# Optimization experiments

Hardware: AMD Instinct MI355X
Metric: run time of the kernel (lower is better)

Reference implementation:

```python
import math
import jax, jax.numpy as jnp
from jax import lax
import numpy as np

PATCHES = [(8, 8), (4, 4), (2, 2), (1, 1)]  # (width, height) per scale
BN_EPS = 1e-5


def setup_inputs() -> dict:
    key = jax.random.key(0)
    ks = jax.random.split(key, 9)
    b, d, h, w = 4, 256, 64, 64
    s = 1.0 / math.sqrt(d)
    return {
        "x": jax.random.normal(ks[0], (b, d, h, w), jnp.float32),
        "wq": jax.random.normal(ks[1], (d, d), jnp.float32) * s,
        "bq": jax.random.normal(ks[2], (d,), jnp.float32) * 0.02,
        "wk": jax.random.normal(ks[3], (d, d), jnp.float32) * s,
        "bk": jax.random.normal(ks[4], (d,), jnp.float32) * 0.02,
        "wv": jax.random.normal(ks[5], (d, d), jnp.float32) * s,
        "bv": jax.random.normal(ks[6], (d,), jnp.float32) * 0.02,
        "w_out": jax.random.normal(ks[7], (d, d, 3, 3), jnp.float32) * (s / 3.0),
        "b_out": jax.random.normal(ks[8], (d,), jnp.float32) * 0.02,
        "gamma": jnp.ones((d,), jnp.float32),
        "beta": jnp.zeros((d,), jnp.float32),
    }


def _to_tokens(t, b, dk, out_h, ph, out_w, pw):
    # [b, dk, h, w] -> [b, out_h*out_w, dk*ph*pw]
    t = t.reshape(b, dk, out_h, ph, out_w, pw)
    t = t.transpose(0, 2, 4, 1, 3, 5)
    return t.reshape(b, out_h * out_w, dk * ph * pw)


def reference(x, wq, bq, wk, bk, wv, bv, w_out, b_out, gamma, beta):
    b, c, h, w = x.shape
    # 1x1 conv projections == channel matmuls
    q = jnp.einsum('bchw,oc->bohw', x, wq) + bq[None, :, None, None]
    k = jnp.einsum('bchw,oc->bohw', x, wk) + bk[None, :, None, None]
    v = jnp.einsum('bchw,oc->bohw', x, wv) + bv[None, :, None, None]

    dk = c // len(PATCHES)
    outs = []
    for i, (pw, ph) in enumerate(PATCHES):
        sl = slice(i * dk, (i + 1) * dk)
        out_h, out_w = h // ph, w // pw
        Q = _to_tokens(q[:, sl], b, dk, out_h, ph, out_w, pw)
        K = _to_tokens(k[:, sl], b, dk, out_h, ph, out_w, pw)
        V = _to_tokens(v[:, sl], b, dk, out_h, ph, out_w, pw)
        scores = jnp.einsum('bnd,bmd->bnm', Q, K) / math.sqrt(Q.shape[-1])
        p = jax.nn.softmax(scores, axis=-1)
        y = jnp.einsum('bnm,bmd->bnd', p, V)
        # tokens -> [b, dk, h, w]
        y = y.reshape(b, out_h, out_w, dk, ph, pw)
        y = y.transpose(0, 3, 1, 4, 2, 5).reshape(b, dk, h, w)
        outs.append(y)
    out = jnp.concatenate(outs, axis=1)

    # 3x3 conv, padding=1
    z = lax.conv_general_dilated(out, w_out, (1, 1), 'SAME',
                                 dimension_numbers=('NCHW', 'OIHW', 'NCHW'))
    z = z + b_out[None, :, None, None]
    # BatchNorm2d (training-mode batch stats)
    mean = jnp.mean(z, axis=(0, 2, 3), keepdims=True)
    var = jnp.var(z, axis=(0, 2, 3), keepdims=True)
    zn = (z - mean) * lax.rsqrt(var + BN_EPS)
    zn = zn * gamma[None, :, None, None] + beta[None, :, None, None]
    # LeakyReLU(0.2)
    return jnp.where(zn > 0, zn, 0.2 * zn)
```

## Files before the change

kernel.cpp:

```cpp
#include <hip/hip_runtime.h>
#include <cmath>


#define OFF_XB  0LL
#define OFF_QB  2097152LL
#define OFF_SS  8388608LL
#define OFF_PP  12582912LL
#define OFF_YT  14680064LL
#define OFF_WQK 18874368LL
#define OFF_BIA 18972672LL
#define OFF_WCV 18973440LL
#define OFF_STT 19268352LL
#define OFF_SP0 19268864LL
#define OFF_S1  19399936LL
#define OFF_P0  19662080LL
#define OFF_P1  19670272LL

#define FC 0.18033688f
#define CSHIFT 6.0f

typedef __attribute__((ext_vector_type(8))) short short8;
typedef __attribute__((ext_vector_type(4))) float f32x4;

__device__ inline unsigned short f2bf(float f) {
  unsigned u = __float_as_uint(f);
  u += 0x7fff + ((u >> 16) & 1);
  return (unsigned short)(u >> 16);
}

__device__ inline unsigned cvt_pk_bf16(float a, float b) {
  unsigned r;
  asm("v_cvt_pk_bf16_f32 %0, %1, %2" : "=v"(r) : "v"(a), "v"(b));
  return r;
}

__global__ __launch_bounds__(256) void prep_k(
    const float* __restrict__ x, unsigned short* __restrict__ xb,
    const float* __restrict__ wq, const float* __restrict__ wk,
    const float* __restrict__ wv, const float* __restrict__ bq,
    const float* __restrict__ bk, const float* __restrict__ bv,
    unsigned short* __restrict__ Wqkv, float* __restrict__ biasQKV,
    const float* __restrict__ wcv, unsigned short* __restrict__ Wcb)
{
  const int bid = blockIdx.x, t = threadIdx.x;
  if (bid < 256) {
    __shared__ unsigned short rowb[256][66];
    const int b = bid >> 6, y = bid & 63;
    for (int i = t; i < 16384; i += 256) {
      int c = i >> 6, xx = i & 63;
      rowb[c][xx] = f2bf(x[((long long)(b*256 + c) << 12) + (y << 6) + xx]);
    }
    __syncthreads();
    unsigned int* outw = (unsigned int*)(xb + ((long long)bid << 14));
    for (int i = t; i < 8192; i += 256) {
      int xx = i >> 7, c2 = (i & 127) * 2;
      outw[xx*128 + (c2 >> 1)] = (unsigned)rowb[c2][xx]
                               | ((unsigned)rowb[c2+1][xx] << 16);
    }
  } else if (bid < 1024) {
    const int row = bid - 256;
    const int which = row >> 8, oc = row & 255;
    const float* src = which == 0 ? wq : which == 1 ? wk : wv;
    Wqkv[row*256 + t] = f2bf(src[oc*256 + t]);
    if (row < 3) {
      const float* bs = row == 0 ? bq : row == 1 ? bk : bv;
      biasQKV[row*256 + t] = bs[t];
    }
  } else {
    int i = (bid - 1024)*256 + t;
    int tap = i >> 16, oc = (i >> 8) & 255, ic = i & 255;
    Wcb[i] = f2bf(wcv[((long long)(oc*256 + ic))*9 + tap]);
  }
}

template<int EPI, int SH = 0>
__device__ void gemm_nt_body(
    const unsigned short* __restrict__ A, const unsigned short* __restrict__ B,
    void* __restrict__ Cv, const float* __restrict__ bias,
    int M, int N, int K, int lda, int ldb, int ldc,
    long long sA, long long sB, long long sC, float alpha,
    int bx, int by, int bz)
{
  const int t = threadIdx.x, l = t & 63;
  const int lr = l & 15, lg = l >> 4;
  const int w = t >> 6, wm = w >> 1, wn = w & 1;
  const int m0 = by*128 + wm*64, n0 = bx*128 + wn*64;
  if (m0 >= M || n0 >= N) return;
  const unsigned short* Ab = A + (long long)bz*sA + (long long)(m0 + lr)*lda + lg*8;
  const unsigned short* Bb = B + (long long)bz*sB + (long long)(n0 + lr)*ldb + lg*8;

  f32x4 acc[4][4] = {};
#pragma unroll 2
  for (int kk = 0; kk < K; kk += 32) {
    short8 af[4], bf[4];
#pragma unroll
    for (int i = 0; i < 4; i++)
      af[i] = *(const short8*)(Ab + (long long)i*16*lda + kk);
#pragma unroll
    for (int i = 0; i < 4; i++)
      bf[i] = *(const short8*)(Bb + (long long)i*16*ldb + kk);
#pragma unroll
    for (int mf = 0; mf < 4; mf++)
#pragma unroll
      for (int nf = 0; nf < 4; nf++)
        acc[mf][nf] = __builtin_amdgcn_mfma_f32_16x16x32_bf16(
            af[mf], bf[nf], acc[mf][nf], 0, 0, 0);
  }

  if (EPI == 0) {
    float* C = (float*)Cv + (long long)bz*sC;
#pragma unroll
    for (int mf = 0; mf < 4; mf++)
#pragma unroll
      for (int r = 0; r < 4; r++) {
        const int row = m0 + mf*16 + lg*4 + r;
#pragma unroll
        for (int nf = 0; nf < 4; nf++)
          C[(long long)row*ldc + n0 + nf*16 + lr] = acc[mf][nf][r] * alpha;
      }
  } else if (EPI == 1) {
    unsigned short* Qbase = (unsigned short*)Cv;
#pragma unroll
    for (int mf = 0; mf < 4; mf++)
#pragma unroll
      for (int r = 0; r < 4; r++) {
        const int gi = m0 + mf*16 + lg*4 + r;
        const int which = gi >> 8, ch = gi & 255;
        const int scale = ch >> 6, c = ch & 63;
        const int sh = 3 - scale, msk = (1 << sh) - 1;
        const bool tr = (which == 2);
        const float bb = bias[gi];
        unsigned short* dst = Qbase + (long long)which*4194304
                            + (long long)scale*1048576 + (long long)bz*262144;
#pragma unroll
        for (int nf = 0; nf < 4; nf++) {
          const int gj = n0 + nf*16 + lr;
          const int y = gj >> 6, xx = gj & 63;
          const int n = (y >> sh)*(64 >> sh) + (xx >> sh);
          const int d = (c << (2*sh)) + ((y & msk) << sh) + (xx & msk);
          const long long idx = tr
              ? (long long)d*(4096 >> (2*sh)) + n
              : (long long)n*(64 << (2*sh)) + d;
          dst[idx] = f2bf(acc[mf][nf][r] + bb);
        }
      }
  } else {
    unsigned short* inb = (unsigned short*)Cv;
    constexpr int msk = (1 << SH) - 1;
    constexpr int scale = 3 - SH;
#pragma unroll
    for (int mf = 0; mf < 4; mf++)
#pragma unroll
      for (int r = 0; r < 4; r++) {
        const int gi = m0 + mf*16 + lg*4 + r;
        const int ty = gi >> (6 - SH), tx = gi & ((64 >> SH) - 1);
#pragma unroll
        for (int nf = 0; nf < 4; nf++) {
          const int gj = n0 + nf*16 + lr;
          const int c = gj >> (2*SH);
          const int y = (ty << SH) | ((gj >> SH) & msk);
          const int x = (tx << SH) | (gj & msk);
          inb[((((long long)bz << 12) + (y << 6) + x) << 8) + scale*64 + c]
              = f2bf(acc[mf][nf][r]);
        }
      }
  }
}

__global__ __launch_bounds__(256) void qkv_k(
    const unsigned short* __restrict__ Wqkv, const unsigned short* __restrict__ xb,
    unsigned short* __restrict__ Qu, const float* __restrict__ biasQKV)
{
  gemm_nt_body<1>(Wqkv, xb, (void*)Qu, biasQKV, 768, 4096, 256, 256, 256, 0,
                  0, 1048576, 0, 1.0f, blockIdx.x, blockIdx.y, blockIdx.z);
}

__device__ void s0_scores_wave(
    const unsigned short* __restrict__ Q, const unsigned short* __restrict__ K,
    float* __restrict__ Sp, int bid)
{
  const int t = threadIdx.x, l = t & 63, w = t >> 6;
  const int lr = l & 15, lg = l >> 4;
  const int task = bid*4 + w;
  const int b = task >> 3, ks = task & 7;
  const unsigned short* Qb = Q + (long long)b*262144;
  const unsigned short* Kb = K + (long long)b*262144;
  f32x4 acc[4][4] = {};
  const int k0 = ks*512;
#pragma unroll 2
  for (int kk = k0; kk < k0 + 512; kk += 32) {
    short8 af[4], bf[4];
#pragma unroll
    for (int i = 0; i < 4; i++)
      af[i] = *(const short8*)(Qb + (long long)(i*16 + lr)*4096 + kk + lg*8);
#pragma unroll
    for (int i = 0; i < 4; i++)
      bf[i] = *(const short8*)(Kb + (long long)(i*16 + lr)*4096 + kk + lg*8);
#pragma unroll
    for (int mf = 0; mf < 4; mf++)
#pragma unroll
      for (int nf = 0; nf < 4; nf++)
        acc[mf][nf] = __builtin_amdgcn_mfma_f32_16x16x32_bf16(
            af[mf], bf[nf], acc[mf][nf], 0, 0, 0);
  }
#pragma unroll
  for (int mf = 0; mf < 4; mf++)
#pragma unroll
    for (int r = 0; r < 4; r++) {
      const int row = mf*16 + lg*4 + r;
#pragma unroll
      for (int nf = 0; nf < 4; nf++)
        Sp[(((long long)(ks*4 + b)*64 + row) << 6) + nf*16 + lr]
            = acc[mf][nf][r];
    }
}

__device__ void flash3_body(
    const unsigned short* __restrict__ Q3, const unsigned short* __restrict__ K3,
    const unsigned short* __restrict__ Vt3, unsigned short* __restrict__ inb,
    int bx, int b)
{
  constexpr int LD = 72;
  __shared__ unsigned short KVs[2][2][64*LD];
  __shared__ unsigned short Ps[64*LD];
  const int t = threadIdx.x, l = t & 63, w = t >> 6;
  const int lr = l & 15, lg = l >> 4;
  const int q0 = bx * 64;
  const long long base = (long long)b * 262144;
  const unsigned short* Qg = Q3 + base;
  const unsigned short* Kg = K3 + base;
  const unsigned short* Vg = Vt3 + base;

  short8 bq[2];
  bq[0] = *(const short8*)(Qg + (long long)(q0 + w*16 + lr)*64 + lg*8);
  bq[1] = *(const short8*)(Qg + (long long)(q0 + w*16 + lr)*64 + 32 + lg*8);

  f32x4 acc[4] = {};
  float li = 0.f;

  const int r_ = t >> 3, c8_ = (t & 7) * 8;
  uint4 kreg[2], vreg[2];

#define LOADKV(KT) do { \
    const int k0_ = (KT) * 64; \
    _Pragma("unroll") \
    for (int it = 0; it < 2; it++) { \
      const int rr = r_ + it*32; \
      kreg[it] = *(const uint4*)(Kg + (long long)(k0_ + rr)*64 + c8_); \
      vreg[it] = *(const uint4*)(Vg + (long long)rr*4096 + k0_ + c8_); \
    } } while (0)
#define STOREKV(BUF) do { \
    _Pragma("unroll") \
    for (int it = 0; it < 2; it++) { \
      const int rr = r_ + it*32; \
      *(uint4*)(KVs[BUF][0] + rr*LD + c8_) = kreg[it]; \
      *(uint4*)(KVs[BUF][1] + rr*LD + c8_) = vreg[it]; \
    } } while (0)

  LOADKV(0);
  STOREKV(0);
  __syncthreads();

  for (int kt = 0; kt < 64; ++kt) {
    if (kt < 63) LOADKV(kt + 1);
    const unsigned short* Ksb = KVs[kt & 1][0];
    const unsigned short* Vsb = KVs[kt & 1][1];
    f32x4 s[4];
#pragma unroll
    for (int cf = 0; cf < 4; cf++) {
      short8 ak0 = *(const short8*)(Ksb + (cf*16 + lr)*LD + lg*8);
      short8 ak1 = *(const short8*)(Ksb + (cf*16 + lr)*LD + 32 + lg*8);
      f32x4 zz = {};
      zz = __builtin_amdgcn_mfma_f32_16x16x32_bf16(ak0, bq[0], zz, 0,0,0);
      s[cf] = __builtin_amdgcn_mfma_f32_16x16x32_bf16(ak1, bq[1], zz, 0,0,0);
    }
    float p[16], psum = 0.f;
#pragma unroll
    for (int cf = 0; cf < 4; cf++)
#pragma unroll
      for (int r = 0; r < 4; r++) {
        float e = exp2f(fmaf(s[cf][r], FC, -CSHIFT));
        p[cf*4 + r] = e; psum += e;
      }
    li += psum;
    {
      unsigned short* pr = Ps + (w*16 + lr)*LD;
#pragma unroll
      for (int cf = 0; cf < 4; cf++) {
        *(unsigned*)(pr + cf*16 + lg*4)     = cvt_pk_bf16(p[cf*4+0], p[cf*4+1]);
        *(unsigned*)(pr + cf*16 + lg*4 + 2) = cvt_pk_bf16(p[cf*4+2], p[cf*4+3]);
      }
    }
    short8 bp0 = *(const short8*)(Ps + (w*16 + lr)*LD + lg*8);
    short8 bp1 = *(const short8*)(Ps + (w*16 + lr)*LD + 32 + lg*8);
#pragma unroll
    for (int df = 0; df < 4; df++) {
      short8 av0 = *(const short8*)(Vsb + (df*16 + lr)*LD + lg*8);
      short8 av1 = *(const short8*)(Vsb + (df*16 + lr)*LD + 32 + lg*8);
      acc[df] = __builtin_amdgcn_mfma_f32_16x16x32_bf16(av0, bp0, acc[df], 0,0,0);
      acc[df] = __builtin_amdgcn_mfma_f32_16x16x32_bf16(av1, bp1, acc[df], 0,0,0);
    }
    if (kt < 63) {
      STOREKV((kt + 1) & 1);
      __syncthreads();
    }
  }
#undef LOADKV
#undef STOREKV
  li += __shfl_xor(li, 16);
  li += __shfl_xor(li, 32);
  const float inv = 1.f / li;
  const long long row = (long long)b*4096 + q0 + w*16 + lr;
  unsigned short* ob = inb + row*256 + 192 + lg*4;
#pragma unroll
  for (int df = 0; df < 4; df++) {
    *(unsigned*)(ob + df*16)     = cvt_pk_bf16(acc[df][0]*inv, acc[df][1]*inv);
    *(unsigned*)(ob + df*16 + 2) = cvt_pk_bf16(acc[df][2]*inv, acc[df][3]*inv);
  }
}

__global__ __launch_bounds__(256) void stageA_k(
    const unsigned short* __restrict__ Qu, const unsigned short* __restrict__ Ku,
    const unsigned short* __restrict__ Vu,
    float* __restrict__ Sp0, float* __restrict__ S1, float* __restrict__ S2,
    unsigned short* __restrict__ inb)
{
  const int bid = blockIdx.x;
  if (bid < 256) {
    flash3_body(Qu+3145728, Ku+3145728, Vu+3145728, inb, bid & 63, bid >> 6);
  } else if (bid < 264) {
    s0_scores_wave(Qu, Ku, Sp0, bid - 256);
  } else if (bid < 280) {
    int q = bid - 264;
    gemm_nt_body<0>(Qu+1048576, Ku+1048576, (void*)S1, nullptr,
        256, 256, 1024, 1024, 1024, 256, 262144, 262144, 65536, 0.03125f,
        q & 1, (q >> 1) & 1, q >> 2);
  } else {
    int q = bid - 280;
    gemm_nt_body<0>(Qu+2097152, Ku+2097152, (void*)S2, nullptr,
        1024, 1024, 256, 256, 256, 1024, 262144, 262144, 1048576, 0.0625f,
        q & 7, (q >> 3) & 7, q >> 6);
  }
}

template<int CNT>
__device__ void softmax_row(const float* __restrict__ S,
                            unsigned short* __restrict__ P, long long row)
{
  const int l = threadIdx.x & 63;
  const float* p = S + row*(CNT*64);
  unsigned short* o = P + row*(CNT*64);
  float v[CNT];
  float mx = -1e30f;
#pragma unroll
  for (int i = 0; i < CNT; i++) { v[i] = p[i*64 + l]; mx = fmaxf(mx, v[i]); }
#pragma unroll
  for (int off = 1; off < 64; off <<= 1) mx = fmaxf(mx, __shfl_xor(mx, off, 64));
  float sum = 0.f;
#pragma unroll
  for (int i = 0; i < CNT; i++) { v[i] = __expf(v[i] - mx); sum += v[i]; }
#pragma unroll
  for (int off = 1; off < 64; off <<= 1) sum += __shfl_xor(sum, off, 64);
  const float inv = 1.f / sum;
#pragma unroll
  for (int i = 0; i < CNT; i++) o[i*64 + l] = f2bf(v[i] * inv);
}

__global__ __launch_bounds__(256) void stageB_k(
    const float* __restrict__ Sp0, unsigned short* __restrict__ P0,
    const float* __restrict__ S1, unsigned short* __restrict__ P1,
    const float* __restrict__ S2, unsigned short* __restrict__ P2)
{
  const int bid = blockIdx.x, t = threadIdx.x, l = t & 63, w = t >> 6;
  if (bid < 1024) {
    softmax_row<16>(S2, P2, (long long)bid*4 + w);
  } else if (bid < 1280) {
    softmax_row<4>(S1, P1, (long long)(bid - 1024)*4 + w);
  } else {
    const int row = (bid - 1280)*4 + w;
    const int b = row >> 6, r = row & 63;
    float v = 0.f;
#pragma unroll
    for (int ks = 0; ks < 8; ks++)
      v += Sp0[(((long long)(ks*4 + b)*64 + r) << 6) + l];
    v *= 0.015625f;
    float mx = v;
#pragma unroll
    for (int off = 1; off < 64; off <<= 1) mx = fmaxf(mx, __shfl_xor(mx, off, 64));
    float e = __expf(v - mx), sum = e;
#pragma unroll
    for (int off = 1; off < 64; off <<= 1) sum += __shfl_xor(sum, off, 64);
    P0[(row << 6) + l] = f2bf(e / sum);
  }
}

__global__ __launch_bounds__(256) void stageC_k(
    const unsigned short* __restrict__ P0, const unsigned short* __restrict__ P1,
    const unsigned short* __restrict__ P2, const unsigned short* __restrict__ Vu,
    unsigned short* __restrict__ inb)
{
  const int bid = blockIdx.x;
  if (bid < 128) {
    int q = bid;
    gemm_nt_body<2,3>(P0, Vu, (void*)inb, nullptr,
        64, 4096, 64, 64, 64, 0, 4096, 262144, 0, 1.0f,
        q & 31, 0, q >> 5);
  } else if (bid < 192) {
    int q = bid - 128;
    gemm_nt_body<2,2>(P1, Vu+1048576, (void*)inb, nullptr,
        256, 1024, 256, 256, 256, 0, 65536, 262144, 0, 1.0f,
        q & 7, (q >> 3) & 1, q >> 4);
  } else {
    int q = bid - 192;
    gemm_nt_body<2,1>(P2, Vu+2097152, (void*)inb, nullptr,
        1024, 256, 1024, 1024, 1024, 0, 1048576, 262144, 0, 1.0f,
        q & 1, (q >> 1) & 7, q >> 4);
  }
}

__global__ __launch_bounds__(512) void conv_mfma_k(
    const unsigned short* __restrict__ inb, const unsigned short* __restrict__ Wb,
    const float* __restrict__ bias, float* __restrict__ z)
{
  __shared__ unsigned short lds[2][6*66*32];
  const int t = threadIdx.x;
  const int l = t & 63, wid = t >> 6;
  const int lr = l & 15, lg = l >> 4;
  const int waveM = wid >> 2, waveN = wid & 3;
  const int b = blockIdx.x >> 4, y0 = (blockIdx.x & 15) * 4;
  const int oc0 = blockIdx.y * 64 + waveM * 32;
  const long long inbase = (long long)b * 1048576;
  const int kgrp = lg * 8;

  f32x4 acc[2][4] = {};
  uint4 sreg[4];

#define CLOAD(IC0) do { \
    _Pragma("unroll") \
    for (int i = 0; i < 4; i++) { \
      int q = t + i*512; \
      if (q < 1584) { \
        int ic8 = q & 3, cc = (q >> 2) % 66, rr = q / 264; \
        int gy = y0 - 1 + rr, gx = cc - 1; \
        uint4 v = make_uint4(0u,0u,0u,0u); \
        if ((unsigned)gy < 64u && (unsigned)gx < 64u) \
          v = *(const uint4*)(inb + inbase + ((long long)(gy*64+gx))*256 \
                              + (IC0) + ic8*8); \
        sreg[i] = v; \
      } \
    } } while (0)
#define CSTORE(BUF) do { \
    _Pragma("unroll") \
    for (int i = 0; i < 4; i++) { \
      int q = t + i*512; \
      if (q < 1584) *(uint4*)(&lds[BUF][q*8]) = sreg[i]; \
    } } while (0)

  CLOAD(0);
  CSTORE(0);
  __syncthreads();

  for (int c = 0; c < 8; ++c) {
    const int ic0 = c * 32;
    if (c < 7) CLOAD(ic0 + 32);
    const unsigned short* wbase = Wb + (long long)(oc0 + lr)*256 + ic0 + kgrp;
    short8 afr[9][2];
#pragma unroll
    for (int tap = 0; tap < 9; tap++) {
      afr[tap][0] = *(const short8*)(wbase + (long long)tap*65536);
      afr[tap][1] = *(const short8*)(wbase + (long long)tap*65536 + 16*256);
    }
    const unsigned short* L = lds[c & 1];
#pragma unroll
    for (int ky = 0; ky < 3; ky++) {
#pragma unroll
      for (int kx = 0; kx < 3; kx++) {
        const int tap = ky*3 + kx;
#pragma unroll
        for (int nf = 0; nf < 4; nf++) {
          int pix = waveN*64 + nf*16 + lr;
          int rp = pix >> 6, xx = pix & 63;
          short8 bf = *(const short8*)(L + ((rp + ky)*66 + xx + kx)*32 + kgrp);
          acc[0][nf] = __builtin_amdgcn_mfma_f32_16x16x32_bf16(
              afr[tap][0], bf, acc[0][nf], 0, 0, 0);
          acc[1][nf] = __builtin_amdgcn_mfma_f32_16x16x32_bf16(
              afr[tap][1], bf, acc[1][nf], 0, 0, 0);
        }
      }
    }
    if (c < 7) {
      CSTORE((c + 1) & 1);
      __syncthreads();
    }
  }
#undef CLOAD
#undef CSTORE

  const long long zb = ((long long)b * 256) << 12;
#pragma unroll
  for (int mf = 0; mf < 2; mf++) {
#pragma unroll
    for (int r = 0; r < 4; r++) {
      const int oc = oc0 + mf*16 + lg*4 + r;
      const float bb = bias[oc];
      const long long rowbase = zb + ((long long)oc << 12) + y0*64;
#pragma unroll
      for (int nf = 0; nf < 4; nf++) {
        int pix = waveN*64 + nf*16 + lr;
        z[rowbase + pix] = acc[mf][nf][r] + bb;
      }
    }
  }
}

__global__ __launch_bounds__(256) void bn_stats_k(
    const float* __restrict__ z, float* __restrict__ stats)
{
  const int ch = blockIdx.x, t = threadIdx.x;
  float s = 0.f, q = 0.f;
  for (int b = 0; b < 4; b++) {
    const float* p = z + ((long long)(b*256 + ch) << 12);
    for (int i = t; i < 4096; i += 256) { float v = p[i]; s += v; q += v*v; }
  }
  __shared__ float rs[256], rq[256];
  rs[t] = s; rq[t] = q; __syncthreads();
  for (int st = 128; st > 0; st >>= 1) {
    if (t < st) { rs[t] += rs[t+st]; rq[t] += rq[t+st]; }
    __syncthreads();
  }
  if (t == 0) {
    float mean = rs[0] * (1.f/16384.f);
    float var  = rq[0] * (1.f/16384.f) - mean*mean;
    stats[ch]       = mean;
    stats[256 + ch] = rsqrtf(var + 1e-5f);
  }
}

__global__ __launch_bounds__(256) void bn_apply_k(
    const float* __restrict__ z, const float* __restrict__ stats,
    const float* __restrict__ gamma, const float* __restrict__ beta,
    float* __restrict__ out)
{
  long long i4 = ((long long)blockIdx.x*256 + threadIdx.x) * 4;
  int ch = (int)((i4 >> 12) & 255);
  float mean = stats[ch], rsg = stats[256 + ch];
  float g = gamma[ch], bt = beta[ch];
  float4 v = *(const float4*)(z + i4);
  float r[4] = {v.x, v.y, v.z, v.w};
#pragma unroll
  for (int j = 0; j < 4; j++) {
    float u = (r[j] - mean) * rsg * g + bt;
    r[j] = u > 0.f ? u : 0.2f * u;
  }
  *(float4*)(out + i4) = make_float4(r[0], r[1], r[2], r[3]);
}

extern "C" void kernel_launch(void* const* d_in, const int* in_sizes, int n_in,
                              void* d_out, int out_size, void* d_ws, size_t ws_size,
                              hipStream_t stream)
{
  const float* x     = (const float*)d_in[0];
  const float* wq    = (const float*)d_in[1];
  const float* bq    = (const float*)d_in[2];
  const float* wk    = (const float*)d_in[3];
  const float* bk    = (const float*)d_in[4];
  const float* wv    = (const float*)d_in[5];
  const float* bv    = (const float*)d_in[6];
  const float* w_out = (const float*)d_in[7];
  const float* b_out = (const float*)d_in[8];
  const float* gamma = (const float*)d_in[9];
  const float* beta  = (const float*)d_in[10];
  float* out = (float*)d_out;

  float* ws = (float*)d_ws;
  unsigned short* xb  = (unsigned short*)(ws + OFF_XB);
  unsigned short* Qu  = (unsigned short*)(ws + OFF_QB);
  unsigned short* Ku  = Qu + 4194304;
  unsigned short* Vu  = Qu + 8388608;
  float* S2  = ws + OFF_SS;
  unsigned short* P2 = (unsigned short*)(ws + OFF_PP);
  unsigned short* Wqk = (unsigned short*)(ws + OFF_WQK);
  float* biasQ = ws + OFF_BIA;
  unsigned short* Wcv = (unsigned short*)(ws + OFF_WCV);
  float* St  = ws + OFF_STT;
  float* Sp0 = ws + OFF_SP0;
  float* S1  = ws + OFF_S1;
  unsigned short* P0 = (unsigned short*)(ws + OFF_P0);
  unsigned short* P1 = (unsigned short*)(ws + OFF_P1);
  unsigned short* inb = (unsigned short*)(ws + OFF_XB);
  float* z = ws + OFF_YT;

  dim3 blk(256);

  prep_k<<<dim3(3328), blk, 0, stream>>>(
      x, xb, wq, wk, wv, bq, bk, bv, Wqk, biasQ, w_out, Wcv);

  qkv_k<<<dim3(32,6,4), blk, 0, stream>>>(Wqk, xb, Qu, biasQ);

  stageA_k<<<dim3(536), blk, 0, stream>>>(Qu, Ku, Vu, Sp0, S1, S2, inb);

  stageB_k<<<dim3(1344), blk, 0, stream>>>(Sp0, P0, S1, P1, S2, P2);

  stageC_k<<<dim3(256), blk, 0, stream>>>(P0, P1, P2, Vu, inb);

  conv_mfma_k<<<dim3(64,4), dim3(512), 0, stream>>>(inb, Wcv, b_out, z);

  bn_stats_k<<<dim3(256), blk, 0, stream>>>(z, St);
  bn_apply_k<<<dim3(4096), blk, 0, stream>>>(z, St, gamma, beta, out);
}
```

Before: 234.3 us.

## Split flash attention keys across four wave groups per block with LDS reduction

The scale-3 flash attention blocks grow from 4 to 16 waves. Each group of 4 waves handles a quarter of the key range, so each wave runs 16 tile iterations instead of 64. Because the softmax uses a fixed exponent shift rather than a running max, partial accumulators and row sums can simply be added. Groups 1-3 write their partials to shared memory and group 0 adds them up and writes the output. This drops the register double-buffered K/V prefetch in favour of plain load-sync-compute steps, and uses much more LDS. Blocks of the other stage-A kinds now launch 1024 threads but exit the extra 768 immediately.

```diff
diff --git a/kernel.cpp b/kernel.cpp
--- a/kernel.cpp
+++ b/kernel.cpp
@@ -221,10 +221,12 @@
     int bx, int b)
 {
   constexpr int LD = 72;
-  __shared__ unsigned short KVs[2][2][64*LD];
-  __shared__ unsigned short Ps[64*LD];
+  __shared__ unsigned short KV4[4][2][64*LD];
+  __shared__ unsigned short Ps4[4][64*LD];
+  __shared__ float liC[192];
   const int t = threadIdx.x, l = t & 63, w = t >> 6;
   const int lr = l & 15, lg = l >> 4;
+  const int grp = w >> 2, sw = w & 3;
   const int q0 = bx * 64;
   const long long base = (long long)b * 262144;
   const unsigned short* Qg = Q3 + base;
@@ -232,44 +234,35 @@
   const unsigned short* Vg = Vt3 + base;
 
   short8 bq[2];
-  bq[0] = *(const short8*)(Qg + (long long)(q0 + w*16 + lr)*64 + lg*8);
-  bq[1] = *(const short8*)(Qg + (long long)(q0 + w*16 + lr)*64 + 32 + lg*8);
+  bq[0] = *(const short8*)(Qg + (long long)(q0 + sw*16 + lr)*64 + lg*8);
+  bq[1] = *(const short8*)(Qg + (long long)(q0 + sw*16 + lr)*64 + 32 + lg*8);
 
   f32x4 acc[4] = {};
   float li = 0.f;
 
-  const int r_ = t >> 3, c8_ = (t & 7) * 8;
-  uint4 kreg[2], vreg[2];
-
-#define LOADKV(KT) do { \
-    const int k0_ = (KT) * 64; \
-    _Pragma("unroll") \
-    for (int it = 0; it < 2; it++) { \
-      const int rr = r_ + it*32; \
-      kreg[it] = *(const uint4*)(Kg + (long long)(k0_ + rr)*64 + c8_); \
-      vreg[it] = *(const uint4*)(Vg + (long long)rr*4096 + k0_ + c8_); \
-    } } while (0)
-#define STOREKV(BUF) do { \
-    _Pragma("unroll") \
-    for (int it = 0; it < 2; it++) { \
-      const int rr = r_ + it*32; \
-      *(uint4*)(KVs[BUF][0] + rr*LD + c8_) = kreg[it]; \
-      *(uint4*)(KVs[BUF][1] + rr*LD + c8_) = vreg[it]; \
-    } } while (0)
-
-  LOADKV(0);
-  STOREKV(0);
-  __syncthreads();
-
-  for (int kt = 0; kt < 64; ++kt) {
-    if (kt < 63) LOADKV(kt + 1);
-    const unsigned short* Ksb = KVs[kt & 1][0];
-    const unsigned short* Vsb = KVs[kt & 1][1];
+  unsigned short* Ks = KV4[grp][0];
+  unsigned short* Vs = KV4[grp][1];
+  unsigned short* Ps = Ps4[grp];
+  const int tg = t & 255;
+  const int r_ = tg >> 3, c8_ = (tg & 7) * 8;
+
+  for (int i = 0; i < 16; i++) {
+    const int k0 = (grp*16 + i) * 64;
+    __syncthreads();
+#pragma unroll
+    for (int it = 0; it < 2; it++) {
+      const int rr = r_ + it*32;
+      *(uint4*)(Ks + rr*LD + c8_) =
+          *(const uint4*)(Kg + (long long)(k0 + rr)*64 + c8_);
+      *(uint4*)(Vs + rr*LD + c8_) =
+          *(const uint4*)(Vg + (long long)rr*4096 + k0 + c8_);
+    }
+    __syncthreads();
     f32x4 s[4];
 #pragma unroll
     for (int cf = 0; cf < 4; cf++) {
-      short8 ak0 = *(const short8*)(Ksb + (cf*16 + lr)*LD + lg*8);
-      short8 ak1 = *(const short8*)(Ksb + (cf*16 + lr)*LD + 32 + lg*8);
+      short8 ak0 = *(const short8*)(Ks + (cf*16 + lr)*LD + lg*8);
+      short8 ak1 = *(const short8*)(Ks + (cf*16 + lr)*LD + 32 + lg*8);
       f32x4 zz = {};
       zz = __builtin_amdgcn_mfma_f32_16x16x32_bf16(ak0, bq[0], zz, 0,0,0);
       s[cf] = __builtin_amdgcn_mfma_f32_16x16x32_bf16(ak1, bq[1], zz, 0,0,0);
@@ -284,42 +277,59 @@
       }
     li += psum;
     {
-      unsigned short* pr = Ps + (w*16 + lr)*LD;
+      unsigned short* pr = Ps + (sw*16 + lr)*LD;
 #pragma unroll
       for (int cf = 0; cf < 4; cf++) {
         *(unsigned*)(pr + cf*16 + lg*4)     = cvt_pk_bf16(p[cf*4+0], p[cf*4+1]);
         *(unsigned*)(pr + cf*16 + lg*4 + 2) = cvt_pk_bf16(p[cf*4+2], p[cf*4+3]);
       }
     }
-    short8 bp0 = *(const short8*)(Ps + (w*16 + lr)*LD + lg*8);
-    short8 bp1 = *(const short8*)(Ps + (w*16 + lr)*LD + 32 + lg*8);
+    short8 bp0 = *(const short8*)(Ps + (sw*16 + lr)*LD + lg*8);
+    short8 bp1 = *(const short8*)(Ps + (sw*16 + lr)*LD + 32 + lg*8);
 #pragma unroll
     for (int df = 0; df < 4; df++) {
-      short8 av0 = *(const short8*)(Vsb + (df*16 + lr)*LD + lg*8);
-      short8 av1 = *(const short8*)(Vsb + (df*16 + lr)*LD + 32 + lg*8);
+      short8 av0 = *(const short8*)(Vs + (df*16 + lr)*LD + lg*8);
+      short8 av1 = *(const short8*)(Vs + (df*16 + lr)*LD + 32 + lg*8);
       acc[df] = __builtin_amdgcn_mfma_f32_16x16x32_bf16(av0, bp0, acc[df], 0,0,0);
       acc[df] = __builtin_amdgcn_mfma_f32_16x16x32_bf16(av1, bp1, acc[df], 0,0,0);
     }
-    if (kt < 63) {
-      STOREKV((kt + 1) & 1);
-      __syncthreads();
-    }
-  }
-#undef LOADKV
-#undef STOREKV
+  }
   li += __shfl_xor(li, 16);
   li += __shfl_xor(li, 32);
-  const float inv = 1.f / li;
-  const long long row = (long long)b*4096 + q0 + w*16 + lr;
-  unsigned short* ob = inb + row*256 + 192 + lg*4;
-#pragma unroll
-  for (int df = 0; df < 4; df++) {
-    *(unsigned*)(ob + df*16)     = cvt_pk_bf16(acc[df][0]*inv, acc[df][1]*inv);
-    *(unsigned*)(ob + df*16 + 2) = cvt_pk_bf16(acc[df][2]*inv, acc[df][3]*inv);
-  }
-}
-
-__global__ __launch_bounds__(256) void stageA_k(
+
+  __syncthreads();
+  float* cb = (float*)KV4;
+  if (grp > 0) {
+    const int slot = (grp - 1)*4 + sw;
+    float* dst = cb + ((long long)slot*64 + l)*17;
+#pragma unroll
+    for (int df = 0; df < 4; df++)
+      *(float4*)(dst + df*4) =
+          make_float4(acc[df][0], acc[df][1], acc[df][2], acc[df][3]);
+    if (lg == 0) liC[slot*16 + lr] = li;
+  }
+  __syncthreads();
+  if (grp == 0) {
+#pragma unroll
+    for (int g2 = 0; g2 < 3; g2++) li += liC[(g2*4 + sw)*16 + lr];
+    const float inv = 1.f / li;
+    const long long row = (long long)b*4096 + q0 + sw*16 + lr;
+    unsigned short* ob = inb + row*256 + 192 + lg*4;
+#pragma unroll
+    for (int df = 0; df < 4; df++) {
+      float r0 = acc[df][0], r1 = acc[df][1], r2 = acc[df][2], r3 = acc[df][3];
+#pragma unroll
+      for (int g2 = 0; g2 < 3; g2++) {
+        float4 v = *(float4*)(cb + ((long long)((g2*4 + sw)*64 + l))*17 + df*4);
+        r0 += v.x; r1 += v.y; r2 += v.z; r3 += v.w;
+      }
+      *(unsigned*)(ob + df*16)     = cvt_pk_bf16(r0*inv, r1*inv);
+      *(unsigned*)(ob + df*16 + 2) = cvt_pk_bf16(r2*inv, r3*inv);
+    }
+  }
+}
+
+__global__ __launch_bounds__(1024) void stageA_k(
     const unsigned short* __restrict__ Qu, const unsigned short* __restrict__ Ku,
     const unsigned short* __restrict__ Vu,
     float* __restrict__ Sp0, float* __restrict__ S1, float* __restrict__ S2,
@@ -328,7 +338,10 @@
   const int bid = blockIdx.x;
   if (bid < 256) {
     flash3_body(Qu+3145728, Ku+3145728, Vu+3145728, inb, bid & 63, bid >> 6);
-  } else if (bid < 264) {
+    return;
+  }
+  if (threadIdx.x >= 256) return;
+  if (bid < 264) {
     s0_scores_wave(Qu, Ku, Sp0, bid - 256);
   } else if (bid < 280) {
     int q = bid - 264;
@@ -597,7 +610,8 @@
 
   qkv_k<<<dim3(32,6,4), blk, 0, stream>>>(Wqk, xb, Qu, biasQ);
 
-  stageA_k<<<dim3(536), blk, 0, stream>>>(Qu, Ku, Vu, Sp0, S1, S2, inb);
+  stageA_k<<<dim3(536), dim3(1024), 0, stream>>>(
+      Qu, Ku, Vu, Sp0, S1, S2, inb);
 
   stageB_k<<<dim3(1344), blk, 0, stream>>>(Sp0, P0, S1, P1, S2, P2);
 
```

Result: slower. 255.1 us (+8.9%).
